# Performance work log

Hardware: AMD Instinct MI355X
Metric: run time of the kernel (lower is better)

The kernel has to match this reference:

```python
import jax, jax.numpy as jnp
import numpy as np

NUM_USERS = 100000
NUM_ITEMS = 50000
IN_DIM = 128
HID_DIM = 256
OUT_DIM = 64
R = 5
E = 300000  # edges per rating level
EPS = 1e-10


def setup_inputs() -> dict:
    key = jax.random.key(0)
    ks = jax.random.split(key, 12)
    # edge lists per rating, regularized to dense [R, E]
    u_idx = jax.random.randint(ks[0], (R, E), 0, NUM_USERS, dtype=jnp.int32)
    v_idx = jax.random.randint(ks[1], (R, E), 0, NUM_ITEMS, dtype=jnp.int32)
    deg_user = jax.random.uniform(ks[2], (NUM_USERS,), dtype=jnp.float32) * 50.0
    deg_item = jax.random.uniform(ks[3], (NUM_ITEMS,), dtype=jnp.float32) * 100.0
    # learned parameters (xavier-ish scaling)
    X_u = jax.random.normal(ks[4], (NUM_USERS, IN_DIM), dtype=jnp.float32) * 0.02
    X_v = jax.random.normal(ks[5], (NUM_ITEMS, IN_DIM), dtype=jnp.float32) * 0.02
    s1 = float(np.sqrt(6.0 / (IN_DIM + HID_DIM)))
    W_item2user = jax.random.uniform(ks[6], (R, IN_DIM, HID_DIM), dtype=jnp.float32, minval=-s1, maxval=s1)
    W_user2item = jax.random.uniform(ks[7], (R, IN_DIM, HID_DIM), dtype=jnp.float32, minval=-s1, maxval=s1)
    s2 = float(np.sqrt(6.0 / (HID_DIM + OUT_DIM)))
    W_out_user = jax.random.uniform(ks[8], (HID_DIM, OUT_DIM), dtype=jnp.float32, minval=-s2, maxval=s2)
    b_out_user = jnp.zeros((OUT_DIM,), dtype=jnp.float32)
    W_out_item = jax.random.uniform(ks[9], (HID_DIM, OUT_DIM), dtype=jnp.float32, minval=-s2, maxval=s2)
    b_out_item = jnp.zeros((OUT_DIM,), dtype=jnp.float32)
    return {
        "u_idx": u_idx, "v_idx": v_idx,
        "deg_user": deg_user, "deg_item": deg_item,
        "X_u": X_u, "X_v": X_v,
        "W_item2user": W_item2user, "W_user2item": W_user2item,
        "W_out_user": W_out_user, "b_out_user": b_out_user,
        "W_out_item": W_out_item, "b_out_item": b_out_item,
    }


def reference(u_idx, v_idx, deg_user, deg_item, X_u, X_v,
              W_item2user, W_user2item,
              W_out_user, b_out_user, W_out_item, b_out_item):
    num_users = X_u.shape[0]
    num_items = X_v.shape[0]
    deg_u = jnp.sqrt(jnp.clip(deg_user, EPS))
    deg_v = jnp.sqrt(jnp.clip(deg_item, EPS))
    # per-edge symmetric normalization, [R, E]
    norm = 1.0 / (deg_u[u_idx] * deg_v[v_idx])
    # gather + per-rating matmul + normalize  ([R,E,in] x [R,in,hid] -> [R,E,hid])
    msgs_to_u = jnp.einsum('rek,rkh->reh', X_v[v_idx], W_item2user) * norm[..., None]
    msgs_to_v = jnp.einsum('rek,rkh->reh', X_u[u_idx], W_user2item) * norm[..., None]
    # scatter-add into shared accumulators (equivalent of index_add_ over all ratings)
    m_u = jax.ops.segment_sum(msgs_to_u.reshape(-1, msgs_to_u.shape[-1]),
                              u_idx.reshape(-1), num_segments=num_users)
    m_v = jax.ops.segment_sum(msgs_to_v.reshape(-1, msgs_to_v.shape[-1]),
                              v_idx.reshape(-1), num_segments=num_items)
    # output dense layers + ReLU (dropout disabled / eval mode)
    h_u = jax.nn.relu(m_u @ W_out_user + b_out_user)
    h_v = jax.nn.relu(m_v @ W_out_item + b_out_item)
    return h_u, h_v
```

## Files before the change

kernel.cpp:

```cpp
#include <hip/hip_runtime.h>
#include <hip/hip_bf16.h>

#define NUM_USERS 100000
#define NUM_ITEMS 50000
#define IN_DIM 128
#define HID_DIM 256
#define OUT_DIM 64
#define R_LEVELS 5
#define NEDGE 300000
#define EPSC 1e-10f

typedef float f32x4 __attribute__((ext_vector_type(4)));
typedef short s16x8 __attribute__((ext_vector_type(8)));

static __device__ __forceinline__ unsigned short f2bf(float f) {
    __hip_bfloat16 h = __float2bfloat16(f);
    return *reinterpret_cast<unsigned short*>(&h);
}

__global__ void fuse_weights(const float* __restrict__ W_i2u,
                             const float* __restrict__ W_u2i,
                             const float* __restrict__ Wout_u,
                             const float* __restrict__ Wout_i,
                             unsigned short* __restrict__ WcT_u,
                             unsigned short* __restrict__ WcT_v) {
    const int rk = blockIdx.x;
    const int r  = rk >> 7;
    const int k  = rk & 127;
    const int j  = threadIdx.x;
    const bool userDir = (blockIdx.y == 0);
    const float* w1   = (userDir ? W_i2u : W_u2i) + (size_t)rk * HID_DIM;
    const float* wout = (userDir ? Wout_u : Wout_i);
    float acc = 0.f;
    for (int h = 0; h < HID_DIM; ++h)
        acc = fmaf(w1[h], wout[h * OUT_DIM + j], acc);
    unsigned short* dst = (userDir ? WcT_u : WcT_v);
    dst[(((size_t)r * OUT_DIM + j) * IN_DIM) + k] = f2bf(acc);
}

__global__ void prescale_rows(const float* __restrict__ X,
                              const float* __restrict__ deg,
                              unsigned short* __restrict__ Xn,
                              float* __restrict__ rsq, int nrows) {
    const int row = blockIdx.x * 4 + (threadIdx.x >> 6);
    if (row >= nrows) return;
    const int lane = threadIdx.x & 63;
    const float r = 1.0f / sqrtf(fmaxf(deg[row], EPSC));
    if (lane == 0) rsq[row] = r;
    const float2 x = ((const float2*)(X + (size_t)row * IN_DIM))[lane];
    const unsigned int packed = (unsigned int)f2bf(x.x * r) |
                                ((unsigned int)f2bf(x.y * r) << 16);
    ((unsigned int*)(Xn + (size_t)row * IN_DIM))[lane] = packed;
}

__global__ __launch_bounds__(256)
void edge_mfma_pre(const int* __restrict__ u_idx,
                   const int* __restrict__ v_idx,
                   const unsigned short* __restrict__ Xn_u,
                   const unsigned short* __restrict__ Xn_v,
                   const unsigned short* __restrict__ WcT_u,
                   const unsigned short* __restrict__ WcT_v,
                   float* __restrict__ out) {
    const int r    = blockIdx.y;
    const bool toUser = (blockIdx.z == 0);
    const int lane = threadIdx.x & 63;
    const int wave = threadIdx.x >> 6;
    const int m    = lane & 15;
    const int g    = lane >> 4;

    const int* dI = (toUser ? u_idx : v_idx) + (size_t)r * NEDGE;
    const int* sI = (toUser ? v_idx : u_idx) + (size_t)r * NEDGE;
    const unsigned short* Xn  = toUser ? Xn_v : Xn_u;
    const unsigned short* WcT = (toUser ? WcT_u : WcT_v) + (size_t)r * OUT_DIM * IN_DIM;
    float* outp = out + (toUser ? 0 : (size_t)NUM_USERS * OUT_DIM);

    s16x8 bfrag[4][4];
#pragma unroll
    for (int nt = 0; nt < 4; ++nt)
#pragma unroll
        for (int ks = 0; ks < 4; ++ks)
            bfrag[nt][ks] = *reinterpret_cast<const s16x8*>(
                WcT + ((size_t)(nt * 16 + m) * IN_DIM + ks * 32 + g * 8));

    const int wid     = blockIdx.x * 4 + wave;
    const int wstride = gridDim.x * 4;
    constexpr int NCHUNK = NEDGE / 16;

    for (int c = wid; c < NCHUNK; c += wstride) {
        const int e0 = c * 16;
        const int sS = sI[e0 + m];
        const int4 dd4 = *reinterpret_cast<const int4*>(dI + e0 + g * 4);
        const unsigned short* xrow = Xn + (size_t)sS * IN_DIM;

        s16x8 afrag[4];
#pragma unroll
        for (int ks = 0; ks < 4; ++ks)
            afrag[ks] = *reinterpret_cast<const s16x8*>(xrow + ks * 32 + g * 8);

        const int dd[4] = {dd4.x, dd4.y, dd4.z, dd4.w};
#pragma unroll
        for (int nt = 0; nt < 4; ++nt) {
            f32x4 acc = {0.f, 0.f, 0.f, 0.f};
#pragma unroll
            for (int ks = 0; ks < 4; ++ks)
                acc = __builtin_amdgcn_mfma_f32_16x16x32_bf16(
                    afrag[ks], bfrag[nt][ks], acc, 0, 0, 0);
#pragma unroll
            for (int i = 0; i < 4; ++i)
                atomicAdd(outp + (size_t)dd[i] * OUT_DIM + nt * 16 + m, acc[i]);
        }
    }
}

__global__ __launch_bounds__(256)
void edge_mfma(const int* __restrict__ u_idx, const int* __restrict__ v_idx,
               const float* __restrict__ deg_user, const float* __restrict__ deg_item,
               const float* __restrict__ X_u, const float* __restrict__ X_v,
               const unsigned short* __restrict__ WcT_u,
               const unsigned short* __restrict__ WcT_v,
               float* __restrict__ out) {
    const int r    = blockIdx.y;
    const bool toUser = (blockIdx.z == 0);
    const int lane = threadIdx.x & 63;
    const int wave = threadIdx.x >> 6;
    const int m    = lane & 15;
    const int g    = lane >> 4;

    const int*   dI   = (toUser ? u_idx : v_idx) + (size_t)r * NEDGE;
    const int*   sI   = (toUser ? v_idx : u_idx) + (size_t)r * NEDGE;
    const float* degD = toUser ? deg_user : deg_item;
    const float* degS = toUser ? deg_item : deg_user;
    const float* Xs   = toUser ? X_v : X_u;
    const unsigned short* WcT = (toUser ? WcT_u : WcT_v) + (size_t)r * OUT_DIM * IN_DIM;
    float* outp = out + (toUser ? 0 : (size_t)NUM_USERS * OUT_DIM);

    s16x8 bfrag[4][4];
#pragma unroll
    for (int nt = 0; nt < 4; ++nt)
#pragma unroll
        for (int ks = 0; ks < 4; ++ks)
            bfrag[nt][ks] = *reinterpret_cast<const s16x8*>(
                WcT + ((size_t)(nt * 16 + m) * IN_DIM + ks * 32 + g * 8));

    const int wid     = blockIdx.x * 4 + wave;
    const int wstride = gridDim.x * 4;
    constexpr int NCHUNK = NEDGE / 16;

    for (int c = wid; c < NCHUNK; c += wstride) {
        const int e0 = c * 16;
        const int sS  = sI[e0 + m];
        const int dDm = dI[e0 + m];
        const float norm = 1.0f / (sqrtf(fmaxf(degD[dDm], EPSC)) *
                                   sqrtf(fmaxf(degS[sS],  EPSC)));
        const float* xrow = Xs + (size_t)sS * IN_DIM;

        s16x8 afrag[4];
#pragma unroll
        for (int ks = 0; ks < 4; ++ks) {
            const float4 q0 = *reinterpret_cast<const float4*>(xrow + ks * 32 + g * 8);
            const float4 q1 = *reinterpret_cast<const float4*>(xrow + ks * 32 + g * 8 + 4);
            s16x8 av;
            av[0] = (short)f2bf(q0.x * norm); av[1] = (short)f2bf(q0.y * norm);
            av[2] = (short)f2bf(q0.z * norm); av[3] = (short)f2bf(q0.w * norm);
            av[4] = (short)f2bf(q1.x * norm); av[5] = (short)f2bf(q1.y * norm);
            av[6] = (short)f2bf(q1.z * norm); av[7] = (short)f2bf(q1.w * norm);
            afrag[ks] = av;
        }

        int dd[4];
#pragma unroll
        for (int i = 0; i < 4; ++i) dd[i] = dI[e0 + g * 4 + i];

#pragma unroll
        for (int nt = 0; nt < 4; ++nt) {
            f32x4 acc = {0.f, 0.f, 0.f, 0.f};
#pragma unroll
            for (int ks = 0; ks < 4; ++ks)
                acc = __builtin_amdgcn_mfma_f32_16x16x32_bf16(
                    afrag[ks], bfrag[nt][ks], acc, 0, 0, 0);
#pragma unroll
            for (int i = 0; i < 4; ++i)
                atomicAdd(outp + (size_t)dd[i] * OUT_DIM + nt * 16 + m, acc[i]);
        }
    }
}

__global__ void bias_relu_scaled(float* __restrict__ out,
                                 const float* __restrict__ b_u,
                                 const float* __restrict__ b_v,
                                 const float* __restrict__ rsq_u,
                                 const float* __restrict__ rsq_v) {
    const size_t i = (size_t)blockIdx.x * 256 + threadIdx.x;
    constexpr size_t UOUT = (size_t)NUM_USERS * OUT_DIM;
    constexpr size_t TOT  = UOUT + (size_t)NUM_ITEMS * OUT_DIM;
    if (i < UOUT) {
        out[i] = fmaxf(fmaf(out[i], rsq_u[i >> 6], b_u[i & 63]), 0.f);
    } else if (i < TOT) {
        const size_t k = i - UOUT;
        out[i] = fmaxf(fmaf(out[i], rsq_v[k >> 6], b_v[i & 63]), 0.f);
    }
}

__global__ void bias_relu(float* __restrict__ out,
                          const float* __restrict__ b_u,
                          const float* __restrict__ b_v) {
    const size_t i = (size_t)blockIdx.x * 256 + threadIdx.x;
    constexpr size_t UOUT = (size_t)NUM_USERS * OUT_DIM;
    constexpr size_t TOT  = UOUT + (size_t)NUM_ITEMS * OUT_DIM;
    if (i < TOT) {
        const float b = (i < UOUT) ? b_u[i & 63] : b_v[i & 63];
        out[i] = fmaxf(out[i] + b, 0.f);
    }
}

extern "C" void kernel_launch(void* const* d_in, const int* in_sizes, int n_in,
                              void* d_out, int out_size, void* d_ws, size_t ws_size,
                              hipStream_t stream) {
    const int*   u_idx    = (const int*)  d_in[0];
    const int*   v_idx    = (const int*)  d_in[1];
    const float* deg_user = (const float*)d_in[2];
    const float* deg_item = (const float*)d_in[3];
    const float* X_u      = (const float*)d_in[4];
    const float* X_v      = (const float*)d_in[5];
    const float* W_i2u    = (const float*)d_in[6];
    const float* W_u2i    = (const float*)d_in[7];
    const float* W_out_u  = (const float*)d_in[8];
    const float* b_out_u  = (const float*)d_in[9];
    const float* W_out_i  = (const float*)d_in[10];
    const float* b_out_i  = (const float*)d_in[11];

    float* out = (float*)d_out;

    constexpr size_t WCT_ELEMS = (size_t)R_LEVELS * OUT_DIM * IN_DIM;
    char* wsb = (char*)d_ws;
    unsigned short* WcT_u = (unsigned short*)wsb;
    unsigned short* WcT_v = WcT_u + WCT_ELEMS;
    float* rsq_u = (float*)(wsb + 163840);
    float* rsq_v = (float*)(wsb + 563840);
    unsigned short* Xn_u = (unsigned short*)(wsb + 763840);
    unsigned short* Xn_v = (unsigned short*)(wsb + 763840 + 25600000);
    constexpr size_t WS_NEED = 763840 + 25600000 + 12800000;
    const bool fast = (ws_size >= WS_NEED);

    hipMemsetAsync(d_out, 0, (size_t)out_size * sizeof(float), stream);

    fuse_weights<<<dim3(R_LEVELS * IN_DIM, 2), 64, 0, stream>>>(
        W_i2u, W_u2i, W_out_u, W_out_i, WcT_u, WcT_v);

    if (fast) {
        prescale_rows<<<(NUM_USERS + 3) / 4, 256, 0, stream>>>(
            X_u, deg_user, Xn_u, rsq_u, NUM_USERS);
        prescale_rows<<<(NUM_ITEMS + 3) / 4, 256, 0, stream>>>(
            X_v, deg_item, Xn_v, rsq_v, NUM_ITEMS);

        edge_mfma_pre<<<dim3(384, R_LEVELS, 2), 256, 0, stream>>>(
            u_idx, v_idx, Xn_u, Xn_v, WcT_u, WcT_v, out);

        const size_t total = (size_t)NUM_USERS * OUT_DIM + (size_t)NUM_ITEMS * OUT_DIM;
        bias_relu_scaled<<<(int)((total + 255) / 256), 256, 0, stream>>>(
            out, b_out_u, b_out_i, rsq_u, rsq_v);
    } else {
        edge_mfma<<<dim3(384, R_LEVELS, 2), 256, 0, stream>>>(
            u_idx, v_idx, deg_user, deg_item, X_u, X_v, WcT_u, WcT_v, out);

        const size_t total = (size_t)NUM_USERS * OUT_DIM + (size_t)NUM_ITEMS * OUT_DIM;
        bias_relu<<<(int)((total + 255) / 256), 256, 0, stream>>>(out, b_out_u, b_out_i);
    }
}
```

Measured before the change: 800.0 us.

## Replace atomic edge scatter with CSR build and per-destination gather-then-matmul

Builds a per-rating CSR (histogram, multi-kernel scan, fill) for both directions and adds a gather kernel. For each destination node it sums the prescaled bf16 source rows per rating in fp32, then applies one MFMA matmul per rating and fuses bias, scaling and ReLU into the store. This avoids per-edge matmuls and float atomics into the output, and drops the memset and the separate bias pass. In exchange it adds several CSR-building launches with integer atomics each call, more workspace, and a warp-divergent gather loop over variable-length neighbor lists. It also rounds the summed features to bf16 before the matmul.

```diff
diff --git a/kernel.cpp b/kernel.cpp
--- a/kernel.cpp
+++ b/kernel.cpp
@@ -9,6 +9,14 @@
 #define R_LEVELS 5
 #define NEDGE 300000
 #define EPSC 1e-10f
+
+#define NE2   (R_LEVELS * NEDGE)
+#define BIN_U (R_LEVELS * NUM_USERS)
+#define BIN_V (R_LEVELS * NUM_ITEMS)
+#define NBIN  (BIN_U + BIN_V)
+#define NLIST (2 * NE2)
+#define SCAN_BLK  2048
+#define SCAN_NBLK ((NBIN + SCAN_BLK - 1) / SCAN_BLK)
 
 typedef float f32x4 __attribute__((ext_vector_type(4)));
 typedef short s16x8 __attribute__((ext_vector_type(8)));
@@ -53,6 +61,176 @@
     ((unsigned int*)(Xn + (size_t)row * IN_DIM))[lane] = packed;
 }
 
+__global__ void hist_kernel(const int* __restrict__ u_idx,
+                            const int* __restrict__ v_idx,
+                            int* __restrict__ cnt) {
+    const int e = blockIdx.x * 256 + threadIdx.x;
+    if (e >= NE2) return;
+    const int r = e / NEDGE;
+    atomicAdd(&cnt[r * NUM_USERS + u_idx[e]], 1);
+    atomicAdd(&cnt[BIN_U + r * NUM_ITEMS + v_idx[e]], 1);
+}
+
+__global__ void scan_local(const int* __restrict__ cnt,
+                           int* __restrict__ off,
+                           int* __restrict__ blksum) {
+    __shared__ int lds[256];
+    const int tid  = threadIdx.x;
+    const int base = blockIdx.x * SCAN_BLK + tid * 8;
+    int v[8]; int s = 0;
+#pragma unroll
+    for (int i = 0; i < 8; ++i) {
+        const int idx = base + i;
+        v[i] = (idx < NBIN) ? cnt[idx] : 0;
+        s += v[i];
+    }
+    lds[tid] = s;
+    __syncthreads();
+    for (int d = 1; d < 256; d <<= 1) {
+        int t = (tid >= d) ? lds[tid - d] : 0;
+        __syncthreads();
+        lds[tid] += t;
+        __syncthreads();
+    }
+    const int inc = lds[tid];
+    if (tid == 255) blksum[blockIdx.x] = inc;
+    int run = inc - s;
+#pragma unroll
+    for (int i = 0; i < 8; ++i) {
+        const int idx = base + i;
+        if (idx < NBIN) off[idx] = run;
+        run += v[i];
+    }
+}
+
+__global__ void scan_top(int* __restrict__ blksum) {
+    __shared__ int lds[512];
+    const int tid = threadIdx.x;
+    const int v = (tid < SCAN_NBLK) ? blksum[tid] : 0;
+    lds[tid] = v;
+    __syncthreads();
+    for (int d = 1; d < 512; d <<= 1) {
+        int t = (tid >= d) ? lds[tid - d] : 0;
+        __syncthreads();
+        lds[tid] += t;
+        __syncthreads();
+    }
+    if (tid < SCAN_NBLK) blksum[tid] = lds[tid] - v;
+}
+
+__global__ void scan_add(int* __restrict__ off, int* __restrict__ cur,
+                         const int* __restrict__ blksum) {
+    const int tid  = threadIdx.x;
+    const int base = blockIdx.x * SCAN_BLK + tid * 8;
+    const int boff = blksum[blockIdx.x];
+#pragma unroll
+    for (int i = 0; i < 8; ++i) {
+        const int idx = base + i;
+        if (idx < NBIN) {
+            const int o = off[idx] + boff;
+            off[idx] = o;
+            cur[idx] = o;
+        }
+    }
+    if (blockIdx.x == 0 && tid == 0) off[NBIN] = NLIST;
+}
+
+__global__ void fill_kernel(const int* __restrict__ u_idx,
+                            const int* __restrict__ v_idx,
+                            int* __restrict__ cur, int* __restrict__ list) {
+    const int e = blockIdx.x * 256 + threadIdx.x;
+    if (e >= NE2) return;
+    const int r = e / NEDGE;
+    const int u = u_idx[e], v = v_idx[e];
+    const int pu = atomicAdd(&cur[r * NUM_USERS + u], 1);
+    list[pu] = v;
+    const int pv = atomicAdd(&cur[BIN_U + r * NUM_ITEMS + v], 1);
+    list[pv] = u;
+}
+
+__global__ __launch_bounds__(256)
+void gather_mfma(const int* __restrict__ off, const int* __restrict__ list,
+                 const unsigned short* __restrict__ Xn_src,
+                 const unsigned short* __restrict__ WcT,
+                 const float* __restrict__ rsq_d,
+                 const float* __restrict__ bias,
+                 float* __restrict__ outp, int nd, int bin_base) {
+    const int lane  = threadIdx.x & 63;
+    const int wave  = threadIdx.x >> 6;
+    const int m     = lane & 15;
+    const int g     = lane >> 4;
+    const int dbase = blockIdx.x * 64 + wave * 16;
+    const int dg    = dbase + m;
+
+    f32x4 accC[4] = {{0.f,0.f,0.f,0.f},{0.f,0.f,0.f,0.f},
+                     {0.f,0.f,0.f,0.f},{0.f,0.f,0.f,0.f}};
+
+    for (int r = 0; r < R_LEVELS; ++r) {
+        int start = 0, len = 0;
+        if (dg < nd) {
+            const int bin = bin_base + r * nd + dg;
+            start = off[bin];
+            len   = off[bin + 1] - start;
+        }
+        float s[4][8];
+#pragma unroll
+        for (int ks = 0; ks < 4; ++ks)
+#pragma unroll
+            for (int i = 0; i < 8; ++i) s[ks][i] = 0.f;
+
+        for (int t = 0; ; ++t) {
+            const bool act = (t < len);
+            if (!__any((int)act)) break;
+            if (act) {
+                const unsigned short* row =
+                    Xn_src + (size_t)list[start + t] * IN_DIM;
+#pragma unroll
+                for (int ks = 0; ks < 4; ++ks) {
+                    const s16x8 w = *reinterpret_cast<const s16x8*>(
+                        row + ks * 32 + g * 8);
+#pragma unroll
+                    for (int i = 0; i < 8; ++i) {
+                        const unsigned int bits =
+                            ((unsigned int)(unsigned short)w[i]) << 16;
+                        s[ks][i] += __uint_as_float(bits);
+                    }
+                }
+            }
+        }
+
+        s16x8 af[4];
+#pragma unroll
+        for (int ks = 0; ks < 4; ++ks)
+#pragma unroll
+            for (int i = 0; i < 8; ++i)
+                af[ks][i] = (short)f2bf(s[ks][i]);
+
+        const unsigned short* Wr = WcT + (size_t)r * OUT_DIM * IN_DIM;
+#pragma unroll
+        for (int nt = 0; nt < 4; ++nt) {
+#pragma unroll
+            for (int ks = 0; ks < 4; ++ks) {
+                const s16x8 bf = *reinterpret_cast<const s16x8*>(
+                    Wr + (size_t)(nt * 16 + m) * IN_DIM + ks * 32 + g * 8);
+                accC[nt] = __builtin_amdgcn_mfma_f32_16x16x32_bf16(
+                    af[ks], bf, accC[nt], 0, 0, 0);
+            }
+        }
+    }
+
+#pragma unroll
+    for (int i = 0; i < 4; ++i) {
+        const int d = dbase + g * 4 + i;
+        if (d < nd) {
+            const float rs = rsq_d[d];
+#pragma unroll
+            for (int nt = 0; nt < 4; ++nt)
+                outp[(size_t)d * OUT_DIM + nt * 16 + m] =
+                    fmaxf(fmaf(accC[nt][i], rs, bias[nt * 16 + m]), 0.f);
+        }
+    }
+}
+
 __global__ __launch_bounds__(256)
 void edge_mfma_pre(const int* __restrict__ u_idx,
                    const int* __restrict__ v_idx,
@@ -112,79 +290,6 @@
     }
 }
 
-__global__ __launch_bounds__(256)
-void edge_mfma(const int* __restrict__ u_idx, const int* __restrict__ v_idx,
-               const float* __restrict__ deg_user, const float* __restrict__ deg_item,
-               const float* __restrict__ X_u, const float* __restrict__ X_v,
-               const unsigned short* __restrict__ WcT_u,
-               const unsigned short* __restrict__ WcT_v,
-               float* __restrict__ out) {
-    const int r    = blockIdx.y;
-    const bool toUser = (blockIdx.z == 0);
-    const int lane = threadIdx.x & 63;
-    const int wave = threadIdx.x >> 6;
-    const int m    = lane & 15;
-    const int g    = lane >> 4;
-
-    const int*   dI   = (toUser ? u_idx : v_idx) + (size_t)r * NEDGE;
-    const int*   sI   = (toUser ? v_idx : u_idx) + (size_t)r * NEDGE;
-    const float* degD = toUser ? deg_user : deg_item;
-    const float* degS = toUser ? deg_item : deg_user;
-    const float* Xs   = toUser ? X_v : X_u;
-    const unsigned short* WcT = (toUser ? WcT_u : WcT_v) + (size_t)r * OUT_DIM * IN_DIM;
-    float* outp = out + (toUser ? 0 : (size_t)NUM_USERS * OUT_DIM);
-
-    s16x8 bfrag[4][4];
-#pragma unroll
-    for (int nt = 0; nt < 4; ++nt)
-#pragma unroll
-        for (int ks = 0; ks < 4; ++ks)
-            bfrag[nt][ks] = *reinterpret_cast<const s16x8*>(
-                WcT + ((size_t)(nt * 16 + m) * IN_DIM + ks * 32 + g * 8));
-
-    const int wid     = blockIdx.x * 4 + wave;
-    const int wstride = gridDim.x * 4;
-    constexpr int NCHUNK = NEDGE / 16;
-
-    for (int c = wid; c < NCHUNK; c += wstride) {
-        const int e0 = c * 16;
-        const int sS  = sI[e0 + m];
-        const int dDm = dI[e0 + m];
-        const float norm = 1.0f / (sqrtf(fmaxf(degD[dDm], EPSC)) *
-                                   sqrtf(fmaxf(degS[sS],  EPSC)));
-        const float* xrow = Xs + (size_t)sS * IN_DIM;
-
-        s16x8 afrag[4];
-#pragma unroll
-        for (int ks = 0; ks < 4; ++ks) {
-            const float4 q0 = *reinterpret_cast<const float4*>(xrow + ks * 32 + g * 8);
-            const float4 q1 = *reinterpret_cast<const float4*>(xrow + ks * 32 + g * 8 + 4);
-            s16x8 av;
-            av[0] = (short)f2bf(q0.x * norm); av[1] = (short)f2bf(q0.y * norm);
-            av[2] = (short)f2bf(q0.z * norm); av[3] = (short)f2bf(q0.w * norm);
-            av[4] = (short)f2bf(q1.x * norm); av[5] = (short)f2bf(q1.y * norm);
-            av[6] = (short)f2bf(q1.z * norm); av[7] = (short)f2bf(q1.w * norm);
-            afrag[ks] = av;
-        }
-
-        int dd[4];
-#pragma unroll
-        for (int i = 0; i < 4; ++i) dd[i] = dI[e0 + g * 4 + i];
-
-#pragma unroll
-        for (int nt = 0; nt < 4; ++nt) {
-            f32x4 acc = {0.f, 0.f, 0.f, 0.f};
-#pragma unroll
-            for (int ks = 0; ks < 4; ++ks)
-                acc = __builtin_amdgcn_mfma_f32_16x16x32_bf16(
-                    afrag[ks], bfrag[nt][ks], acc, 0, 0, 0);
-#pragma unroll
-            for (int i = 0; i < 4; ++i)
-                atomicAdd(outp + (size_t)dd[i] * OUT_DIM + nt * 16 + m, acc[i]);
-        }
-    }
-}
-
 __global__ void bias_relu_scaled(float* __restrict__ out,
                                  const float* __restrict__ b_u,
                                  const float* __restrict__ b_v,
@@ -198,18 +303,6 @@
     } else if (i < TOT) {
         const size_t k = i - UOUT;
         out[i] = fmaxf(fmaf(out[i], rsq_v[k >> 6], b_v[i & 63]), 0.f);
-    }
-}
-
-__global__ void bias_relu(float* __restrict__ out,
-                          const float* __restrict__ b_u,
-                          const float* __restrict__ b_v) {
-    const size_t i = (size_t)blockIdx.x * 256 + threadIdx.x;
-    constexpr size_t UOUT = (size_t)NUM_USERS * OUT_DIM;
-    constexpr size_t TOT  = UOUT + (size_t)NUM_ITEMS * OUT_DIM;
-    if (i < TOT) {
-        const float b = (i < UOUT) ? b_u[i & 63] : b_v[i & 63];
-        out[i] = fmaxf(out[i] + b, 0.f);
     }
 }
 
@@ -230,40 +323,51 @@
     const float* b_out_i  = (const float*)d_in[11];
 
     float* out = (float*)d_out;
-
-    constexpr size_t WCT_ELEMS = (size_t)R_LEVELS * OUT_DIM * IN_DIM;
-    char* wsb = (char*)d_ws;
-    unsigned short* WcT_u = (unsigned short*)wsb;
-    unsigned short* WcT_v = WcT_u + WCT_ELEMS;
-    float* rsq_u = (float*)(wsb + 163840);
-    float* rsq_v = (float*)(wsb + 563840);
-    unsigned short* Xn_u = (unsigned short*)(wsb + 763840);
-    unsigned short* Xn_v = (unsigned short*)(wsb + 763840 + 25600000);
-    constexpr size_t WS_NEED = 763840 + 25600000 + 12800000;
-    const bool fast = (ws_size >= WS_NEED);
-
-    hipMemsetAsync(d_out, 0, (size_t)out_size * sizeof(float), stream);
+    char*  wsb = (char*)d_ws;
+
+    size_t o = 0;
+    unsigned short* WcT_u = (unsigned short*)(wsb + o); o += 81920;
+    unsigned short* WcT_v = (unsigned short*)(wsb + o); o += 81920;
+    float* rsq_u = (float*)(wsb + o); o += 400000;
+    float* rsq_v = (float*)(wsb + o); o += 200000;
+    unsigned short* Xn_u = (unsigned short*)(wsb + o); o += 25600000;
+    unsigned short* Xn_v = (unsigned short*)(wsb + o); o += 12800000;
+    const size_t WS_FAST = o;
+    int* cnt    = (int*)(wsb + o); o += (size_t)NBIN * 4;
+    int* off    = (int*)(wsb + o); o += 3000064;
+    int* cur    = (int*)(wsb + o); o += (size_t)NBIN * 4;
+    int* blksum = (int*)(wsb + o); o += 2048;
+    int* list   = (int*)(wsb + o); o += (size_t)NLIST * 4;
+    const size_t WS_CSR = o;
+    const bool csr = (ws_size >= WS_CSR);
+    (void)WS_FAST;
 
     fuse_weights<<<dim3(R_LEVELS * IN_DIM, 2), 64, 0, stream>>>(
         W_i2u, W_u2i, W_out_u, W_out_i, WcT_u, WcT_v);
-
-    if (fast) {
-        prescale_rows<<<(NUM_USERS + 3) / 4, 256, 0, stream>>>(
-            X_u, deg_user, Xn_u, rsq_u, NUM_USERS);
-        prescale_rows<<<(NUM_ITEMS + 3) / 4, 256, 0, stream>>>(
-            X_v, deg_item, Xn_v, rsq_v, NUM_ITEMS);
-
+    prescale_rows<<<(NUM_USERS + 3) / 4, 256, 0, stream>>>(
+        X_u, deg_user, Xn_u, rsq_u, NUM_USERS);
+    prescale_rows<<<(NUM_ITEMS + 3) / 4, 256, 0, stream>>>(
+        X_v, deg_item, Xn_v, rsq_v, NUM_ITEMS);
+
+    if (csr) {
+        hipMemsetAsync(cnt, 0, (size_t)NBIN * 4, stream);
+        hist_kernel<<<(NE2 + 255) / 256, 256, 0, stream>>>(u_idx, v_idx, cnt);
+        scan_local<<<SCAN_NBLK, 256, 0, stream>>>(cnt, off, blksum);
+        scan_top<<<1, 512, 0, stream>>>(blksum);
+        scan_add<<<SCAN_NBLK, 256, 0, stream>>>(off, cur, blksum);
+        fill_kernel<<<(NE2 + 255) / 256, 256, 0, stream>>>(u_idx, v_idx, cur, list);
+
+        gather_mfma<<<(NUM_USERS + 63) / 64, 256, 0, stream>>>(
+            off, list, Xn_v, WcT_u, rsq_u, b_out_u, out, NUM_USERS, 0);
+        gather_mfma<<<(NUM_ITEMS + 63) / 64, 256, 0, stream>>>(
+            off, list, Xn_u, WcT_v, rsq_v, b_out_i,
+            out + (size_t)NUM_USERS * OUT_DIM, NUM_ITEMS, BIN_U);
+    } else {
+        hipMemsetAsync(d_out, 0, (size_t)out_size * sizeof(float), stream);
         edge_mfma_pre<<<dim3(384, R_LEVELS, 2), 256, 0, stream>>>(
             u_idx, v_idx, Xn_u, Xn_v, WcT_u, WcT_v, out);
-
         const size_t total = (size_t)NUM_USERS * OUT_DIM + (size_t)NUM_ITEMS * OUT_DIM;
         bias_relu_scaled<<<(int)((total + 255) / 256), 256, 0, stream>>>(
             out, b_out_u, b_out_i, rsq_u, rsq_v);
-    } else {
-        edge_mfma<<<dim3(384, R_LEVELS, 2), 256, 0, stream>>>(
-            u_idx, v_idx, deg_user, deg_item, X_u, X_v, WcT_u, WcT_v, out);
-
-        const size_t total = (size_t)NUM_USERS * OUT_DIM + (size_t)NUM_ITEMS * OUT_DIM;
-        bias_relu<<<(int)((total + 255) / 256), 256, 0, stream>>>(out, b_out_u, b_out_i);
-    }
-}
+    }
+}
```

Measured after the change: 779.3 us. 1.03x faster.
